# Optimization experiments

Hardware: AMD Instinct MI355X
Metric: run time of the kernel (lower is better)

The kernel has to match this reference:

```python
import jax, jax.numpy as jnp
import numpy as np

B, L, D, N = 2, 2048, 1024, 16
HD = D // N  # head_dim = 64
EPS = 1e-5


def layer_norm(x, gamma, beta):
    mu = jnp.mean(x, axis=-1, keepdims=True)
    var = jnp.mean(jnp.square(x - mu), axis=-1, keepdims=True)
    return (x - mu) * jax.lax.rsqrt(var + EPS) * gamma + beta


def setup_inputs() -> dict:
    key = jax.random.key(0)
    ks = jax.random.split(key, 10)
    s = lambda fan_in: 1.0 / np.sqrt(fan_in)
    return {
        "x": jax.random.normal(ks[0], (B, L, D), dtype=jnp.float32),
        "wq": jax.random.uniform(ks[1], (D, D), jnp.float32, -s(D), s(D)),
        "wk": jax.random.uniform(ks[2], (D, D), jnp.float32, -s(D), s(D)),  # shared w_proj (k and v)
        "wo": jax.random.uniform(ks[3], (D, D), jnp.float32, -s(D), s(D)),
        "g1": jnp.ones((D,), jnp.float32),
        "b1": jnp.zeros((D,), jnp.float32),
        "w1": jax.random.uniform(ks[4], (D, 4 * D), jnp.float32, -s(D), s(D)),
        "bb1": jax.random.uniform(ks[5], (4 * D,), jnp.float32, -s(D), s(D)),
        "w2": jax.random.uniform(ks[6], (4 * D, D), jnp.float32, -s(4 * D), s(4 * D)),
        "bb2": jax.random.uniform(ks[7], (D,), jnp.float32, -s(4 * D), s(4 * D)),
        "g2": jnp.ones((D,), jnp.float32),
        "b2": jnp.zeros((D,), jnp.float32),
    }


def reference(x, wq, wk, wo, g1, b1, w1, bb1, w2, bb2, g2, b2):
    b, l, d = x.shape
    # projections (w_proj is shared for k and v in the source; v output is unused)
    q = (x @ wq).reshape(b, l, HD, N)
    k = (x @ wk).reshape(b, l, HD, N)
    # attention scores [b, l, m, n]; softmax over m (dim=2 in source)
    scores = jnp.einsum('bldn,bmdn->blmn', q, k) / np.sqrt(HD).astype(np.float32)
    attn = jax.nn.softmax(scores, axis=2)
    # NOTE: source contracts attention weights with K, not V (faithful bug reproduction)
    ctx = jnp.einsum('blmn,bmdn->bldn', attn, k).reshape(b, l, d)
    attn_out = ctx @ wo
    # post-LN residual block
    h = layer_norm(x + attn_out, g1, b1)
    ff = jax.nn.gelu(h @ w1 + bb1, approximate=False) @ w2 + bb2
    return layer_norm(h + ff, g2, b2)
```

## Files before the change

### kernel.cpp

```cpp
#include <hip/hip_runtime.h>
#include <math.h>

typedef unsigned short u16;
typedef unsigned int u32;
typedef __bf16 bf16x8 __attribute__((ext_vector_type(8)));
typedef unsigned short us8 __attribute__((ext_vector_type(8)));
typedef unsigned short us4 __attribute__((ext_vector_type(4)));
typedef float f32x4 __attribute__((ext_vector_type(4)));

#define DEV __device__ __forceinline__

DEV float fast_exp2(float x) { return __builtin_amdgcn_exp2f(x); }

DEV u16 f2bf(float f) {
  __bf16 h = (__bf16)f;
  return __builtin_bit_cast(u16, h);
}
DEV float bf2f(u16 h) { return __builtin_bit_cast(float, (u32)h << 16); }

DEV bf16x8 ld_bf8(const u16* p) { return __builtin_bit_cast(bf16x8, *(const us8*)p); }

DEV void gload_lds16(const u16* g, u16* l) {
  __builtin_amdgcn_global_load_lds((const __attribute__((address_space(1))) void*)g,
                                   (__attribute__((address_space(3))) void*)l, 16, 0, 0);
}

DEV f32x4 mfma16(bf16x8 a, bf16x8 b, f32x4 c) {
  return __builtin_amdgcn_mfma_f32_16x16x32_bf16(a, b, c, 0, 0, 0);
}

DEV float fast_gelu(float u) {
  const float e = fast_exp2(-u * (2.3022048f + 0.10294343f * u * u));
  return u / (1.f + e);
}

#define BAR __builtin_amdgcn_s_barrier()
#define LGK asm volatile("s_waitcnt lgkmcnt(0)" ::: "memory")
#define VM4 asm volatile("s_waitcnt vmcnt(4)" ::: "memory")


__global__ void conv_bf16_kernel(const float* __restrict__ in, u16* __restrict__ out, int n4) {
  const int stride = gridDim.x * blockDim.x;
  for (int i = blockIdx.x * blockDim.x + threadIdx.x; i < n4; i += stride) {
    float4 v = ((const float4*)in)[i];
    us4 h; h[0] = f2bf(v.x); h[1] = f2bf(v.y); h[2] = f2bf(v.z); h[3] = f2bf(v.w);
    ((us4*)out)[i] = h;
  }
}

template <int P>
__global__ __launch_bounds__(256) void transpose_bf16_kernel(
    const float* __restrict__ in, u16* __restrict__ out, int K, int N, float scale) {
  __shared__ float tile[32][33];
  const int nbk = K >> 5;
  const int bk = blockIdx.x % nbk, bn = blockIdx.x / nbk;
  const int r0 = bk << 5, c0 = bn << 5;
  const int t = threadIdx.x;
  {
    const int r = t >> 3, c4 = (t & 7) << 2;
    int sr = r0 + r;
    if constexpr (P == 2) sr = ((sr & 63) << 4) | (sr >> 6);
    const float4 v = *(const float4*)(in + (size_t)sr * N + c0 + c4);
    tile[r][c4] = v.x; tile[r][c4 + 1] = v.y; tile[r][c4 + 2] = v.z; tile[r][c4 + 3] = v.w;
  }
  __syncthreads();
  {
    const int oc = t >> 3, r4 = (t & 7) << 2;
    int orow = c0 + oc;
    if constexpr (P == 1) orow = ((orow & 15) << 6) | (orow >> 4);
    us4 h;
#pragma unroll
    for (int j = 0; j < 4; j++) h[j] = f2bf(tile[r4 + j][oc] * scale);
    *(us4*)(out + (size_t)orow * K + r0 + r4) = h;
  }
}

__global__ __launch_bounds__(256) void khead_transpose(
    const u16* __restrict__ qk, u16* __restrict__ kth) {
  __shared__ u16 tT[64 * 64];
  char* base = (char*)tT;
  const int t = threadIdx.x;
  const int bid = blockIdx.x;
  const int lt = bid & 31, n = (bid >> 5) & 15, b = bid >> 9;
#pragma unroll
  for (int rr = 0; rr < 2; rr++) {
    const int l = rr * 32 + (t >> 3);
    const int d0 = (t & 7) * 8;
    us8 v = *(const us8*)(qk + ((size_t)(b * 2048 + lt * 64 + l)) * 2048 + 1024 + n * 64 + d0);
#pragma unroll
    for (int j = 0; j < 8; j++) {
      const int d = d0 + j;
      *(u16*)(base + d * 128 + ((2 * l) ^ (16 * (d >> 3)))) = v[j];
    }
  }
  __syncthreads();
  const int w = t >> 6, lane = t & 63;
#pragma unroll
  for (int rr = 0; rr < 2; rr++) {
    const int d = rr * 32 + w * 8 + (lane >> 3);
    const int l = (lane & 7) * 8;
    us8 v = *(const us8*)(base + d * 128 + ((2 * l) ^ (16 * (d >> 3))));
    *(us8*)(kth + ((size_t)((b * 16 + n) * 64 + d)) * 2048 + lt * 64 + l) = v;
  }
}

template <int MODE, int BN>
__global__ __launch_bounds__(256) void gemm128(
    const u16* __restrict__ A, const u16* __restrict__ BT,
    int M, int N, int K,
    u16* __restrict__ ob, float* __restrict__ of, const float* __restrict__ res) {
  constexpr int NJ = BN / 32;
  constexpr int WCC = BN / 2;
  __shared__ u16 As[2][4096];
  __shared__ u16 Bs[2][BN * 32];
  const int t = threadIdx.x;
  const int nbm = M >> 7;
  const int nblk = nbm * (N / BN);
  int bid = blockIdx.x;
  bid = (bid & 7) * (nblk >> 3) + (bid >> 3);
  const int bm = bid % nbm;
  const int bn = bid / nbm;
  const int m0 = bm << 7, n0 = bn * BN;
  const int w = t >> 6, lane = t & 63;
  const int wr = w >> 1, wc = w & 1;
  const int lr = lane & 15, lg = lane >> 4, lq = (lane >> 4) << 2;
  const int rsw = (lg ^ (lr & 3)) << 3;

  const int srow = t >> 2;
  const int sseg = (t & 3) ^ (srow & 3);
  const u16* ap = A + (size_t)(m0 + srow) * K + sseg * 8;
  const u16* bp = BT + (size_t)(n0 + srow) * K + sseg * 8;
  const size_t half = (size_t)64 * K;

#define STAGE(buf, k0)                                                 \
  {                                                                    \
    gload_lds16(ap + (k0), &As[buf][t << 3]);                          \
    gload_lds16(ap + half + (k0), &As[buf][(t << 3) + 2048]);          \
    gload_lds16(bp + (k0), &Bs[buf][t << 3]);                          \
    if constexpr (BN == 128)                                           \
      gload_lds16(bp + half + (k0), &Bs[buf][(t << 3) + 2048]);        \
  }

  f32x4 acc[4][NJ];
#pragma unroll
  for (int i = 0; i < 4; i++)
#pragma unroll
    for (int j = 0; j < NJ; j++) acc[i][j] = (f32x4){0.f, 0.f, 0.f, 0.f};

  STAGE(0, 0);
  __syncthreads();
  const int NI = K >> 5;
  for (int it = 0; it < NI; ++it) {
    const int buf = it & 1;
    if (it + 1 < NI) STAGE(buf ^ 1, (it + 1) << 5);
    bf16x8 af[4], bfr[NJ];
#pragma unroll
    for (int i = 0; i < 4; i++)
      af[i] = ld_bf8(&As[buf][(wr * 64 + i * 16 + lr) * 32 + rsw]);
#pragma unroll
    for (int j = 0; j < NJ; j++)
      bfr[j] = ld_bf8(&Bs[buf][(wc * WCC + j * 16 + lr) * 32 + rsw]);
#pragma unroll
    for (int i = 0; i < 4; i++)
#pragma unroll
      for (int j = 0; j < NJ; j++) acc[i][j] = mfma16(af[i], bfr[j], acc[i][j]);
    __syncthreads();
  }
#undef STAGE

#pragma unroll
  for (int i = 0; i < 4; i++) {
    const int r0 = m0 + wr * 64 + i * 16 + lq;
#pragma unroll
    for (int j = 0; j < NJ; j++) {
      const int c = n0 + wc * WCC + j * 16 + lr;
      if constexpr (MODE == 0) {
#pragma unroll
        for (int q = 0; q < 4; q++) ob[(size_t)(r0 + q) * N + c] = f2bf(acc[i][j][q]);
      } else {
#pragma unroll
        for (int q = 0; q < 4; q++) {
          const size_t idx = (size_t)(r0 + q) * N + c;
          of[idx] = acc[i][j][q] + res[idx];
        }
      }
    }
  }
}

template <int MODE, int KS>
__global__ __launch_bounds__(512, 2) void gemm256(
    const u16* __restrict__ A, const u16* __restrict__ BT,
    int M, int N, int K,
    u16* __restrict__ ob, float* __restrict__ of, const float* __restrict__ bias) {
  __shared__ u16 AL[2][2][8192];
  __shared__ u16 BL[2][2][8192];
  const int t = threadIdx.x;
  const int lane = t & 63, wid = t >> 6;
  const int lr = lane & 15, lg = lane >> 4;
  const int wm = wid >> 2, wn = wid & 3;
  const int nbm = M >> 8, nbn = N >> 8;
  const int nblk = nbm * nbn * KS;
  int bid = blockIdx.x;
  bid = (bid & 7) * (nblk >> 3) + (bid >> 3);
  int ks = 0;
  if constexpr (KS > 1) { ks = bid % KS; bid /= KS; }
  const int bm = bid % nbm, bn = bid / nbm;
  const int m0 = bm << 8, n0 = bn << 8;
  const int KB = K / KS;
  const int NT = KB >> 6;
  const u16* Ag = A + (size_t)m0 * K + ks * KB;
  const u16* Bg = BT + (size_t)n0 * K + ks * KB;
  const int sseg = (t & 7) ^ ((t >> 3) & 7);
  const int akey = lr & 7;

  auto stgA = [&](int buf, int h, int kt) {
    const u16* s = Ag + (size_t)(h * 128 + (t >> 3)) * K + kt * 64 + sseg * 8;
    gload_lds16(s, &AL[buf][h][t * 8]);
    gload_lds16(s + (size_t)64 * K, &AL[buf][h][4096 + t * 8]);
  };
  auto stgB = [&](int buf, int h, int kt) {
    const u16* s = Bg + (size_t)(h * 128 + (t >> 3)) * K + kt * 64 + sseg * 8;
    gload_lds16(s, &BL[buf][h][t * 8]);
    gload_lds16(s + (size_t)64 * K, &BL[buf][h][4096 + t * 8]);
  };

#define RDA(DST, BUF, IB)                                                      \
  _Pragma("unroll") for (int i4 = 0; i4 < 4; i4++)                             \
  _Pragma("unroll") for (int kk = 0; kk < 2; kk++)                             \
    DST[i4][kk] = ld_bf8(&AL[BUF][wm][((IB + i4) * 16 + lr) * 64 +             \
                                      ((kk * 4 + lg) ^ akey) * 8]);
#define RDB(DST, BUF, JB)                                                      \
  _Pragma("unroll") for (int j2 = 0; j2 < 2; j2++)                             \
  _Pragma("unroll") for (int kk = 0; kk < 2; kk++)                             \
    DST[j2][kk] = ld_bf8(&BL[BUF][wn >> 1][((wn & 1) * 64 + (JB + j2) * 16 +   \
                                            lr) * 64 +                         \
                                           ((kk * 4 + lg) ^ akey) * 8]);
#define QUAD(AF, BF, IB, JB)                                                   \
  __builtin_amdgcn_s_setprio(1);                                               \
  _Pragma("unroll") for (int i4 = 0; i4 < 4; i4++)                             \
  _Pragma("unroll") for (int j2 = 0; j2 < 2; j2++)                             \
  _Pragma("unroll") for (int kk = 0; kk < 2; kk++)                             \
    acc[IB + i4][JB + j2] = mfma16(AF[i4][kk], BF[j2][kk], acc[IB + i4][JB + j2]); \
  __builtin_amdgcn_s_setprio(0);

  f32x4 acc[8][4];
#pragma unroll
  for (int i = 0; i < 8; i++)
#pragma unroll
    for (int j = 0; j < 4; j++) acc[i][j] = (f32x4){0.f, 0.f, 0.f, 0.f};
  bf16x8 a0[4][2], a1[4][2], b0[2][2], b1[2][2];

  stgA(0, 0, 0); stgA(0, 1, 0); stgB(0, 0, 0); stgB(0, 1, 0);
  stgA(1, 0, 1); stgA(1, 1, 1);
  VM4;
  BAR;

  const int NI = NT >> 1;
  for (int it = 0; it < NI; ++it) {
    const int kt1 = 2 * it + 1;
    const int ktA = (2 * it + 2 < NT) ? 2 * it + 2 : NT - 1;
    const int ktB = (2 * it + 3 < NT) ? 2 * it + 3 : NT - 1;
    RDA(a0, 0, 0); RDB(b0, 0, 0); stgB(1, 0, kt1);
    BAR; QUAD(a0, b0, 0, 0); LGK; BAR;
    RDA(a1, 0, 4); stgB(1, 1, kt1);
    BAR; QUAD(a1, b0, 4, 0); LGK; BAR;
    RDB(b1, 0, 2); stgA(0, 0, ktA);
    BAR; QUAD(a1, b1, 4, 2); LGK; BAR;
    stgA(0, 1, ktA);
    BAR; QUAD(a0, b1, 0, 2); LGK; VM4; BAR;
    RDA(a0, 1, 0); RDB(b0, 1, 0); stgB(0, 0, ktA);
    BAR; QUAD(a0, b0, 0, 0); LGK; BAR;
    RDA(a1, 1, 4); stgB(0, 1, ktA);
    BAR; QUAD(a1, b0, 4, 0); LGK; BAR;
    RDB(b1, 1, 2); stgA(1, 0, ktB);
    BAR; QUAD(a1, b1, 4, 2); LGK; BAR;
    stgA(1, 1, ktB);
    BAR; QUAD(a0, b1, 0, 2); LGK; VM4; BAR;
  }
#undef RDA
#undef RDB
#undef QUAD

#pragma unroll
  for (int i = 0; i < 8; i++) {
    const int r = m0 + wm * 128 + i * 16 + lg * 4;
#pragma unroll
    for (int j = 0; j < 4; j++) {
      const int c = n0 + wn * 64 + j * 16 + lr;
      if constexpr (MODE == 0) {
        const float bv = bias[c];
#pragma unroll
        for (int q = 0; q < 4; q++)
          ob[(size_t)(r + q) * N + c] = f2bf(fast_gelu(acc[i][j][q] + bv));
      } else if constexpr (MODE == 1) {
        u16* op = ob + (size_t)ks * M * N;
#pragma unroll
        for (int q = 0; q < 4; q++) op[(size_t)(r + q) * N + c] = f2bf(acc[i][j][q]);
      } else {
#pragma unroll
        for (int q = 0; q < 4; q++) ob[(size_t)(r + q) * N + c] = f2bf(acc[i][j][q]);
      }
    }
  }
}

__global__ __launch_bounds__(256, 4) void attn_kernel(
    const u16* __restrict__ qk, const u16* __restrict__ kth,
    u16* __restrict__ op, float* __restrict__ stat) {
  __shared__ u16 KsB[2][4096];
  __shared__ u16 KtsB[2][4096];
  __shared__ u16 Plds[4][1024];
  const int t = threadIdx.x, w = t >> 6, lane = t & 63;
  const int lr = lane & 15, lg = lane >> 4;
  int bid = blockIdx.x;
  bid = (bid & 7) * 128 + (bid >> 3);
  const int kv = bid & 1, qb = (bid >> 1) & 15, hn = (bid >> 5) & 15, b = bid >> 9;
  const int lw = qb * 128 + w * 32;
  const int m00 = kv * 1024;
  const u16* ksrc = qk + (size_t)b * 2048 * 2048 + 1024 + hn * 64;
  const u16* ktb = kth + ((size_t)(b * 16 + hn)) * 64 * 2048;
  char* pb = (char*)&Plds[w][0];
  const int swz = (lr & 7) << 4;

#define STAGE_KV(buf, m0s)                                                    \
  {                                                                           \
    _Pragma("unroll") for (int i_ = 0; i_ < 2; i_++) {                        \
      const int s_ = t + 256 * i_;                                            \
      const int row_ = s_ >> 3;                                               \
      const int c_ = (s_ & 7) ^ (row_ & 7);                                   \
      gload_lds16(ksrc + (size_t)((m0s) + row_) * 2048 + c_ * 8,              \
                  &KsB[buf][s_ * 8]);                                         \
      gload_lds16(ktb + (size_t)row_ * 2048 + (m0s) + c_ * 8,                 \
                  &KtsB[buf][s_ * 8]);                                        \
    }                                                                         \
  }

  bf16x8 qf[2][2];
#pragma unroll
  for (int f = 0; f < 2; f++)
#pragma unroll
    for (int kk = 0; kk < 2; kk++)
      qf[f][kk] = ld_bf8(qk + (size_t)(b * 2048 + lw + 16 * f + lr) * 2048 + hn * 64 +
                         kk * 32 + lg * 8);

  float lrow[2] = {0.f, 0.f};
  f32x4 o[2][4];
#pragma unroll
  for (int f = 0; f < 2; f++)
#pragma unroll
    for (int dj = 0; dj < 4; dj++) o[f][dj] = (f32x4){0.f, 0.f, 0.f, 0.f};

  STAGE_KV(0, m00);
  __syncthreads();

  for (int it = 0; it < 16; ++it) {
    const int buf = it & 1;
    if (it < 15) STAGE_KV(buf ^ 1, m00 + (it + 1) * 64);

    f32x4 sc[2][4];
#pragma unroll
    for (int f = 0; f < 2; f++)
#pragma unroll
      for (int mj = 0; mj < 4; mj++) sc[f][mj] = (f32x4){0.f, 0.f, 0.f, 0.f};
#pragma unroll
    for (int mj = 0; mj < 4; mj++) {
      const int krow = 16 * mj + lr;
      bf16x8 kf0 = ld_bf8(&KsB[buf][krow * 64 + ((lg ^ (krow & 7)) << 3)]);
      bf16x8 kf1 = ld_bf8(&KsB[buf][krow * 64 + (((4 + lg) ^ (krow & 7)) << 3)]);
#pragma unroll
      for (int f = 0; f < 2; f++) {
        sc[f][mj] = mfma16(kf0, qf[f][0], sc[f][mj]);
        sc[f][mj] = mfma16(kf1, qf[f][1], sc[f][mj]);
      }
    }

    bf16x8 pa[2][2];
#pragma unroll
    for (int f = 0; f < 2; f++) {
      float ts = 0.f;
#pragma unroll
      for (int mj = 0; mj < 4; mj++) {
        float p0 = fast_exp2(sc[f][mj][0]);
        float p1 = fast_exp2(sc[f][mj][1]);
        float p2 = fast_exp2(sc[f][mj][2]);
        float p3 = fast_exp2(sc[f][mj][3]);
        ts += (p0 + p1) + (p2 + p3);
        u32 w0 = (u32)f2bf(p0) | ((u32)f2bf(p1) << 16);
        u32 w1 = (u32)f2bf(p2) | ((u32)f2bf(p3) << 16);
        *(uint2*)(pb + ((lr * 128 + mj * 32 + lg * 8) ^ swz)) = make_uint2(w0, w1);
      }
      lrow[f] += ts;
#pragma unroll
      for (int kk = 0; kk < 2; kk++)
        pa[f][kk] = __builtin_bit_cast(
            bf16x8, *(const us8*)(pb + ((lr * 128 + kk * 64 + lg * 16) ^ swz)));
    }

#pragma unroll
    for (int dj = 0; dj < 4; dj++) {
      const int vrow = dj * 16 + lr;
      bf16x8 v0 = ld_bf8(&KtsB[buf][vrow * 64 + ((lg ^ (vrow & 7)) << 3)]);
      bf16x8 v1 = ld_bf8(&KtsB[buf][vrow * 64 + (((4 + lg) ^ (vrow & 7)) << 3)]);
#pragma unroll
      for (int f = 0; f < 2; f++) {
        o[f][dj] = mfma16(pa[f][0], v0, o[f][dj]);
        o[f][dj] = mfma16(pa[f][1], v1, o[f][dj]);
      }
    }
    __syncthreads();
  }
#undef STAGE_KV

  u16* ob = op + (size_t)kv * 4096 * 1024;
#pragma unroll
  for (int f = 0; f < 2; f++) {
    lrow[f] += __shfl_xor(lrow[f], 16);
    lrow[f] += __shfl_xor(lrow[f], 32);
#pragma unroll
    for (int q = 0; q < 4; q++) {
      const int ll = lw + 16 * f + 4 * lg + q;
#pragma unroll
      for (int dj = 0; dj < 4; dj++) {
        ob[((size_t)(b * 2048 + ll)) * 1024 + hn * 64 + dj * 16 + lr] = f2bf(o[f][dj][q]);
      }
    }
    if (lg == 0) {
      const int sidx = (b * 16 + hn) * 2048 + lw + 16 * f + lr;
      stat[kv * 65536 + sidx] = lrow[f];
    }
  }
}

__global__ __launch_bounds__(256) void attn_combine(
    const u16* __restrict__ op, const float* __restrict__ stat, u16* __restrict__ ctxh) {
  const int row = blockIdx.x, t = threadIdx.x;
  const int hn = t >> 4;
  const int b = row >> 11, l = row & 2047;
  const int sidx = (b * 16 + hn) * 2048 + l;
  const float inv = 1.f / (stat[sidx] + stat[65536 + sidx]);
  const us4 a = *(const us4*)(op + (size_t)row * 1024 + t * 4);
  const us4 c = *(const us4*)(op + (size_t)(4096 + row) * 1024 + t * 4);
  us4 h;
#pragma unroll
  for (int j = 0; j < 4; j++) h[j] = f2bf((bf2f(a[j]) + bf2f(c[j])) * inv);
  *(us4*)(ctxh + (size_t)row * 1024 + t * 4) = h;
}

__global__ __launch_bounds__(256) void ln1_kernel(
    const float* __restrict__ in, const float* __restrict__ gamma,
    const float* __restrict__ beta, u16* __restrict__ o16) {
  __shared__ float red[8];
  const int row = blockIdx.x, t = threadIdx.x;
  const float4 v = ((const float4*)(in + (size_t)row * 1024))[t];
  float s = v.x + v.y + v.z + v.w;
  float ss = v.x * v.x + v.y * v.y + v.z * v.z + v.w * v.w;
#pragma unroll
  for (int off = 1; off < 64; off <<= 1) { s += __shfl_xor(s, off); ss += __shfl_xor(ss, off); }
  if ((t & 63) == 0) { red[t >> 6] = s; red[4 + (t >> 6)] = ss; }
  __syncthreads();
  const float st = red[0] + red[1] + red[2] + red[3];
  const float sst = red[4] + red[5] + red[6] + red[7];
  const float mean = st * (1.f / 1024.f);
  const float var = sst * (1.f / 1024.f) - mean * mean;
  const float rs = rsqrtf(var + 1e-5f);
  const float4 gv = ((const float4*)gamma)[t];
  const float4 bv = ((const float4*)beta)[t];
  us4 h;
  h[0] = f2bf((v.x - mean) * rs * gv.x + bv.x);
  h[1] = f2bf((v.y - mean) * rs * gv.y + bv.y);
  h[2] = f2bf((v.z - mean) * rs * gv.z + bv.z);
  h[3] = f2bf((v.w - mean) * rs * gv.w + bv.w);
  *(us4*)(o16 + (size_t)row * 1024 + t * 4) = h;
}

template <int NP>
__global__ __launch_bounds__(256) void ln2_kernel(
    const u16* __restrict__ p, size_t pstride,
    const u16* __restrict__ resb, const float* __restrict__ bias,
    const float* __restrict__ gamma, const float* __restrict__ beta,
    float* __restrict__ o32) {
  __shared__ float red[8];
  const int row = blockIdx.x, t = threadIdx.x;
  float4 v;
  {
    const float4 vb = ((const float4*)bias)[t];
    const us4 rb = *(const us4*)(resb + (size_t)row * 1024 + t * 4);
    v.x = bf2f(rb[0]) + vb.x;
    v.y = bf2f(rb[1]) + vb.y;
    v.z = bf2f(rb[2]) + vb.z;
    v.w = bf2f(rb[3]) + vb.w;
  }
#pragma unroll
  for (int k = 0; k < NP; k++) {
    const us4 pv = *(const us4*)(p + (size_t)k * pstride + (size_t)row * 1024 + t * 4);
    v.x += bf2f(pv[0]); v.y += bf2f(pv[1]); v.z += bf2f(pv[2]); v.w += bf2f(pv[3]);
  }
  float s = v.x + v.y + v.z + v.w;
  float ss = v.x * v.x + v.y * v.y + v.z * v.z + v.w * v.w;
#pragma unroll
  for (int off = 1; off < 64; off <<= 1) { s += __shfl_xor(s, off); ss += __shfl_xor(ss, off); }
  if ((t & 63) == 0) { red[t >> 6] = s; red[4 + (t >> 6)] = ss; }
  __syncthreads();
  const float st = red[0] + red[1] + red[2] + red[3];
  const float sst = red[4] + red[5] + red[6] + red[7];
  const float mean = st * (1.f / 1024.f);
  const float var = sst * (1.f / 1024.f) - mean * mean;
  const float rs = rsqrtf(var + 1e-5f);
  const float4 gv = ((const float4*)gamma)[t];
  const float4 bv = ((const float4*)beta)[t];
  float4 ov;
  ov.x = (v.x - mean) * rs * gv.x + bv.x;
  ov.y = (v.y - mean) * rs * gv.y + bv.y;
  ov.z = (v.z - mean) * rs * gv.z + bv.z;
  ov.w = (v.w - mean) * rs * gv.w + bv.w;
  ((float4*)(o32 + (size_t)row * 1024))[t] = ov;
}

extern "C" void kernel_launch(void* const* d_in, const int* in_sizes, int n_in,
                              void* d_out, int out_size, void* d_ws, size_t ws_size,
                              hipStream_t stream) {
  const float* x   = (const float*)d_in[0];
  const float* wq  = (const float*)d_in[1];
  const float* wk  = (const float*)d_in[2];
  const float* wo  = (const float*)d_in[3];
  const float* g1  = (const float*)d_in[4];
  const float* b1  = (const float*)d_in[5];
  const float* w1  = (const float*)d_in[6];
  const float* bb1 = (const float*)d_in[7];
  const float* w2  = (const float*)d_in[8];
  const float* bb2 = (const float*)d_in[9];
  const float* g2  = (const float*)d_in[10];
  const float* b2  = (const float*)d_in[11];

  char* ws = (char*)d_ws;
  const size_t MB = 1ull << 20;
  u16* w2T   = (u16*)(ws + 0 * MB);
  u16* hb    = (u16*)(ws + 8 * MB);
  u16* obuf  = (u16*)(ws + 16 * MB);
  float* stat = (float*)(ws + 32 * MB);
  u16* tbuf  = (u16*)(ws + 16 * MB);
  u16* rA16  = (u16*)(ws + 48 * MB);
  u16* wqkT  = (u16*)(ws + 26 * MB);
  u16* xb    = (u16*)(ws + 33 * MB);
  u16* qk    = (u16*)(ws + 41 * MB);
  u16* kthp  = (u16*)(ws + 57 * MB);
  u16* ctxh  = (u16*)(ws + 65 * MB);
  float* rbuf = (float*)(ws + 73 * MB);
  u16* w1T   = (u16*)(ws + 89 * MB);
  u16* woT   = (u16*)(ws + 97 * MB);

  conv_bf16_kernel<<<1024, 256, 0, stream>>>(x, xb, 1048576);
  transpose_bf16_kernel<1><<<1024, 256, 0, stream>>>(wq, wqkT, 1024, 1024, 0.125f * 1.44269504089f);
  transpose_bf16_kernel<1><<<1024, 256, 0, stream>>>(wk, wqkT + (size_t)1024 * 1024, 1024, 1024, 1.0f);
  transpose_bf16_kernel<2><<<1024, 256, 0, stream>>>(wo, woT, 1024, 1024, 1.0f);
  transpose_bf16_kernel<0><<<32 * 128, 256, 0, stream>>>(w1, w1T, 1024, 4096, 1.0f);
  transpose_bf16_kernel<0><<<128 * 32, 256, 0, stream>>>(w2, w2T, 4096, 1024, 1.0f);

  gemm256<2, 1><<<128, 512, 0, stream>>>(xb, wqkT, 4096, 2048, 1024, qk, nullptr, nullptr);
  khead_transpose<<<1024, 256, 0, stream>>>(qk, kthp);

  attn_kernel<<<1024, 256, 0, stream>>>(qk, kthp, obuf, stat);
  attn_combine<<<4096, 256, 0, stream>>>(obuf, stat, ctxh);

  gemm128<2, 64><<<32 * 16, 256, 0, stream>>>(ctxh, woT, 4096, 1024, 1024, nullptr, rbuf, x);
  ln1_kernel<<<4096, 256, 0, stream>>>(rbuf, g1, b1, hb);

  gemm256<0, 1><<<256, 512, 0, stream>>>(hb, w1T, 4096, 4096, 1024, tbuf, nullptr, bb1);
  const size_t MN = (size_t)4096 * 1024;
  gemm256<1, 4><<<256, 512, 0, stream>>>(tbuf, w2T, 4096, 1024, 4096, rA16, nullptr, nullptr);
  ln2_kernel<4><<<4096, 256, 0, stream>>>(rA16, MN, hb, bb2, g2, b2, (float*)d_out);
}
```

Before: 243.1 us.

## Split-K QK and Wo GEMMs, fold partial sums into consumers, MFMA row sums

The QK projection GEMM now uses 2-way split-K with bf16 partials, which khead_transpose and attn_kernel sum on load. khead_transpose also writes a contiguous per-head K copy. The Wo GEMM moves from the 128-tile kernel to the 256-tile kernel with 4-way split-K, and ln1 sums the partials plus the fp32 residual. Attention row sums are computed with an MFMA against a ones vector instead of scalar adds and shuffles, and priority hints bracket the MFMA sections. The aim is better GPU occupancy on small-grid GEMMs, at the cost of extra partial-buffer traffic and bf16 rounding of the partials.

```diff
diff --git a/kernel.cpp b/kernel.cpp
--- a/kernel.cpp
+++ b/kernel.cpp
@@ -76,9 +76,10 @@
 }
 
 __global__ __launch_bounds__(256) void khead_transpose(
-    const u16* __restrict__ qk, u16* __restrict__ kth) {
+    const u16* __restrict__ qkP, u16* __restrict__ kth, u16* __restrict__ ksum) {
   __shared__ u16 tT[64 * 64];
   char* base = (char*)tT;
+  const size_t PS = (size_t)4096 * 2048;
   const int t = threadIdx.x;
   const int bid = blockIdx.x;
   const int lt = bid & 31, n = (bid >> 5) & 15, b = bid >> 9;
@@ -86,11 +87,17 @@
   for (int rr = 0; rr < 2; rr++) {
     const int l = rr * 32 + (t >> 3);
     const int d0 = (t & 7) * 8;
-    us8 v = *(const us8*)(qk + ((size_t)(b * 2048 + lt * 64 + l)) * 2048 + 1024 + n * 64 + d0);
+    const size_t idx = ((size_t)(b * 2048 + lt * 64 + l)) * 2048 + 1024 + n * 64 + d0;
+    us8 va = *(const us8*)(qkP + idx);
+    us8 vb = *(const us8*)(qkP + PS + idx);
+    us8 sm;
+#pragma unroll
+    for (int j = 0; j < 8; j++) sm[j] = f2bf(bf2f(va[j]) + bf2f(vb[j]));
+    *(us8*)(ksum + (((size_t)(b * 16 + n) * 2048 + lt * 64 + l)) * 64 + d0) = sm;
 #pragma unroll
     for (int j = 0; j < 8; j++) {
       const int d = d0 + j;
-      *(u16*)(base + d * 128 + ((2 * l) ^ (16 * (d >> 3)))) = v[j];
+      *(u16*)(base + d * 128 + ((2 * l) ^ (16 * (d >> 3)))) = sm[j];
     }
   }
   __syncthreads();
@@ -104,95 +111,11 @@
   }
 }
 
-template <int MODE, int BN>
-__global__ __launch_bounds__(256) void gemm128(
-    const u16* __restrict__ A, const u16* __restrict__ BT,
-    int M, int N, int K,
-    u16* __restrict__ ob, float* __restrict__ of, const float* __restrict__ res) {
-  constexpr int NJ = BN / 32;
-  constexpr int WCC = BN / 2;
-  __shared__ u16 As[2][4096];
-  __shared__ u16 Bs[2][BN * 32];
-  const int t = threadIdx.x;
-  const int nbm = M >> 7;
-  const int nblk = nbm * (N / BN);
-  int bid = blockIdx.x;
-  bid = (bid & 7) * (nblk >> 3) + (bid >> 3);
-  const int bm = bid % nbm;
-  const int bn = bid / nbm;
-  const int m0 = bm << 7, n0 = bn * BN;
-  const int w = t >> 6, lane = t & 63;
-  const int wr = w >> 1, wc = w & 1;
-  const int lr = lane & 15, lg = lane >> 4, lq = (lane >> 4) << 2;
-  const int rsw = (lg ^ (lr & 3)) << 3;
-
-  const int srow = t >> 2;
-  const int sseg = (t & 3) ^ (srow & 3);
-  const u16* ap = A + (size_t)(m0 + srow) * K + sseg * 8;
-  const u16* bp = BT + (size_t)(n0 + srow) * K + sseg * 8;
-  const size_t half = (size_t)64 * K;
-
-#define STAGE(buf, k0)                                                 \
-  {                                                                    \
-    gload_lds16(ap + (k0), &As[buf][t << 3]);                          \
-    gload_lds16(ap + half + (k0), &As[buf][(t << 3) + 2048]);          \
-    gload_lds16(bp + (k0), &Bs[buf][t << 3]);                          \
-    if constexpr (BN == 128)                                           \
-      gload_lds16(bp + half + (k0), &Bs[buf][(t << 3) + 2048]);        \
-  }
-
-  f32x4 acc[4][NJ];
-#pragma unroll
-  for (int i = 0; i < 4; i++)
-#pragma unroll
-    for (int j = 0; j < NJ; j++) acc[i][j] = (f32x4){0.f, 0.f, 0.f, 0.f};
-
-  STAGE(0, 0);
-  __syncthreads();
-  const int NI = K >> 5;
-  for (int it = 0; it < NI; ++it) {
-    const int buf = it & 1;
-    if (it + 1 < NI) STAGE(buf ^ 1, (it + 1) << 5);
-    bf16x8 af[4], bfr[NJ];
-#pragma unroll
-    for (int i = 0; i < 4; i++)
-      af[i] = ld_bf8(&As[buf][(wr * 64 + i * 16 + lr) * 32 + rsw]);
-#pragma unroll
-    for (int j = 0; j < NJ; j++)
-      bfr[j] = ld_bf8(&Bs[buf][(wc * WCC + j * 16 + lr) * 32 + rsw]);
-#pragma unroll
-    for (int i = 0; i < 4; i++)
-#pragma unroll
-      for (int j = 0; j < NJ; j++) acc[i][j] = mfma16(af[i], bfr[j], acc[i][j]);
-    __syncthreads();
-  }
-#undef STAGE
-
-#pragma unroll
-  for (int i = 0; i < 4; i++) {
-    const int r0 = m0 + wr * 64 + i * 16 + lq;
-#pragma unroll
-    for (int j = 0; j < NJ; j++) {
-      const int c = n0 + wc * WCC + j * 16 + lr;
-      if constexpr (MODE == 0) {
-#pragma unroll
-        for (int q = 0; q < 4; q++) ob[(size_t)(r0 + q) * N + c] = f2bf(acc[i][j][q]);
-      } else {
-#pragma unroll
-        for (int q = 0; q < 4; q++) {
-          const size_t idx = (size_t)(r0 + q) * N + c;
-          of[idx] = acc[i][j][q] + res[idx];
-        }
-      }
-    }
-  }
-}
-
 template <int MODE, int KS>
 __global__ __launch_bounds__(512, 2) void gemm256(
     const u16* __restrict__ A, const u16* __restrict__ BT,
     int M, int N, int K,
-    u16* __restrict__ ob, float* __restrict__ of, const float* __restrict__ bias) {
+    u16* __restrict__ ob, const float* __restrict__ bias) {
   __shared__ u16 AL[2][2][8192];
   __shared__ u16 BL[2][2][8192];
   const int t = threadIdx.x;
@@ -293,24 +216,22 @@
 #pragma unroll
         for (int q = 0; q < 4; q++)
           ob[(size_t)(r + q) * N + c] = f2bf(fast_gelu(acc[i][j][q] + bv));
-      } else if constexpr (MODE == 1) {
+      } else {
         u16* op = ob + (size_t)ks * M * N;
 #pragma unroll
         for (int q = 0; q < 4; q++) op[(size_t)(r + q) * N + c] = f2bf(acc[i][j][q]);
-      } else {
-#pragma unroll
-        for (int q = 0; q < 4; q++) ob[(size_t)(r + q) * N + c] = f2bf(acc[i][j][q]);
       }
     }
   }
 }
 
 __global__ __launch_bounds__(256, 4) void attn_kernel(
-    const u16* __restrict__ qk, const u16* __restrict__ kth,
-    u16* __restrict__ op, float* __restrict__ stat) {
+    const u16* __restrict__ qkP, const u16* __restrict__ ksum,
+    const u16* __restrict__ kth, u16* __restrict__ op, float* __restrict__ stat) {
   __shared__ u16 KsB[2][4096];
   __shared__ u16 KtsB[2][4096];
   __shared__ u16 Plds[4][1024];
+  const size_t PS = (size_t)4096 * 2048;
   const int t = threadIdx.x, w = t >> 6, lane = t & 63;
   const int lr = lane & 15, lg = lane >> 4;
   int bid = blockIdx.x;
@@ -318,7 +239,7 @@
   const int kv = bid & 1, qb = (bid >> 1) & 15, hn = (bid >> 5) & 15, b = bid >> 9;
   const int lw = qb * 128 + w * 32;
   const int m00 = kv * 1024;
-  const u16* ksrc = qk + (size_t)b * 2048 * 2048 + 1024 + hn * 64;
+  const u16* ksrc = ksum + ((size_t)(b * 16 + hn)) * 2048 * 64;
   const u16* ktb = kth + ((size_t)(b * 16 + hn)) * 64 * 2048;
   char* pb = (char*)&Plds[w][0];
   const int swz = (lr & 7) << 4;
@@ -329,7 +250,7 @@
       const int s_ = t + 256 * i_;                                            \
       const int row_ = s_ >> 3;                                               \
       const int c_ = (s_ & 7) ^ (row_ & 7);                                   \
-      gload_lds16(ksrc + (size_t)((m0s) + row_) * 2048 + c_ * 8,              \
+      gload_lds16(ksrc + (size_t)((m0s) + row_) * 64 + c_ * 8,                \
                   &KsB[buf][s_ * 8]);                                         \
       gload_lds16(ktb + (size_t)row_ * 2048 + (m0s) + c_ * 8,                 \
                   &KtsB[buf][s_ * 8]);                                        \
@@ -340,16 +261,30 @@
 #pragma unroll
   for (int f = 0; f < 2; f++)
 #pragma unroll
-    for (int kk = 0; kk < 2; kk++)
-      qf[f][kk] = ld_bf8(qk + (size_t)(b * 2048 + lw + 16 * f + lr) * 2048 + hn * 64 +
-                         kk * 32 + lg * 8);
-
-  float lrow[2] = {0.f, 0.f};
+    for (int kk = 0; kk < 2; kk++) {
+      const size_t qi = (size_t)(b * 2048 + lw + 16 * f + lr) * 2048 + hn * 64 +
+                        kk * 32 + lg * 8;
+      us8 qa = *(const us8*)(qkP + qi);
+      us8 qb2 = *(const us8*)(qkP + PS + qi);
+      us8 qs;
+#pragma unroll
+      for (int j = 0; j < 8; j++) qs[j] = f2bf(bf2f(qa[j]) + bf2f(qb2[j]));
+      qf[f][kk] = __builtin_bit_cast(bf16x8, qs);
+    }
+
+  us8 ou;
+#pragma unroll
+  for (int j = 0; j < 8; j++) ou[j] = 0x3f80;
+  const bf16x8 ones = __builtin_bit_cast(bf16x8, ou);
+
+  f32x4 ol[2];
   f32x4 o[2][4];
 #pragma unroll
-  for (int f = 0; f < 2; f++)
+  for (int f = 0; f < 2; f++) {
+    ol[f] = (f32x4){0.f, 0.f, 0.f, 0.f};
 #pragma unroll
     for (int dj = 0; dj < 4; dj++) o[f][dj] = (f32x4){0.f, 0.f, 0.f, 0.f};
+  }
 
   STAGE_KV(0, m00);
   __syncthreads();
@@ -363,6 +298,7 @@
     for (int f = 0; f < 2; f++)
 #pragma unroll
       for (int mj = 0; mj < 4; mj++) sc[f][mj] = (f32x4){0.f, 0.f, 0.f, 0.f};
+    __builtin_amdgcn_s_setprio(1);
 #pragma unroll
     for (int mj = 0; mj < 4; mj++) {
       const int krow = 16 * mj + lr;
@@ -374,29 +310,30 @@
         sc[f][mj] = mfma16(kf1, qf[f][1], sc[f][mj]);
       }
     }
+    __builtin_amdgcn_s_setprio(0);
 
     bf16x8 pa[2][2];
 #pragma unroll
     for (int f = 0; f < 2; f++) {
-      float ts = 0.f;
 #pragma unroll
       for (int mj = 0; mj < 4; mj++) {
         float p0 = fast_exp2(sc[f][mj][0]);
         float p1 = fast_exp2(sc[f][mj][1]);
         float p2 = fast_exp2(sc[f][mj][2]);
         float p3 = fast_exp2(sc[f][mj][3]);
-        ts += (p0 + p1) + (p2 + p3);
         u32 w0 = (u32)f2bf(p0) | ((u32)f2bf(p1) << 16);
         u32 w1 = (u32)f2bf(p2) | ((u32)f2bf(p3) << 16);
         *(uint2*)(pb + ((lr * 128 + mj * 32 + lg * 8) ^ swz)) = make_uint2(w0, w1);
       }
-      lrow[f] += ts;
 #pragma unroll
       for (int kk = 0; kk < 2; kk++)
         pa[f][kk] = __builtin_bit_cast(
             bf16x8, *(const us8*)(pb + ((lr * 128 + kk * 64 + lg * 16) ^ swz)));
-    }
-
+      ol[f] = mfma16(pa[f][0], ones, ol[f]);
+      ol[f] = mfma16(pa[f][1], ones, ol[f]);
+    }
+
+    __builtin_amdgcn_s_setprio(1);
 #pragma unroll
     for (int dj = 0; dj < 4; dj++) {
       const int vrow = dj * 16 + lr;
@@ -408,6 +345,7 @@
         o[f][dj] = mfma16(pa[f][1], v1, o[f][dj]);
       }
     }
+    __builtin_amdgcn_s_setprio(0);
     __syncthreads();
   }
 #undef STAGE_KV
@@ -415,8 +353,6 @@
   u16* ob = op + (size_t)kv * 4096 * 1024;
 #pragma unroll
   for (int f = 0; f < 2; f++) {
-    lrow[f] += __shfl_xor(lrow[f], 16);
-    lrow[f] += __shfl_xor(lrow[f], 32);
 #pragma unroll
     for (int q = 0; q < 4; q++) {
       const int ll = lw + 16 * f + 4 * lg + q;
@@ -425,9 +361,10 @@
         ob[((size_t)(b * 2048 + ll)) * 1024 + hn * 64 + dj * 16 + lr] = f2bf(o[f][dj][q]);
       }
     }
-    if (lg == 0) {
-      const int sidx = (b * 16 + hn) * 2048 + lw + 16 * f + lr;
-      stat[kv * 65536 + sidx] = lrow[f];
+    if (lr == 0) {
+      const int sb = (b * 16 + hn) * 2048 + lw + 16 * f + 4 * lg;
+#pragma unroll
+      for (int q = 0; q < 4; q++) stat[kv * 65536 + sb + q] = ol[f][q];
     }
   }
 }
@@ -448,11 +385,17 @@
 }
 
 __global__ __launch_bounds__(256) void ln1_kernel(
-    const float* __restrict__ in, const float* __restrict__ gamma,
-    const float* __restrict__ beta, u16* __restrict__ o16) {
+    const u16* __restrict__ p, size_t pstride, const float* __restrict__ xres,
+    const float* __restrict__ gamma, const float* __restrict__ beta,
+    u16* __restrict__ o16) {
   __shared__ float red[8];
   const int row = blockIdx.x, t = threadIdx.x;
-  const float4 v = ((const float4*)(in + (size_t)row * 1024))[t];
+  float4 v = ((const float4*)(xres + (size_t)row * 1024))[t];
+#pragma unroll
+  for (int k = 0; k < 4; k++) {
+    const us4 pv = *(const us4*)(p + (size_t)k * pstride + (size_t)row * 1024 + t * 4);
+    v.x += bf2f(pv[0]); v.y += bf2f(pv[1]); v.z += bf2f(pv[2]); v.w += bf2f(pv[3]);
+  }
   float s = v.x + v.y + v.z + v.w;
   float ss = v.x * v.x + v.y * v.y + v.z * v.z + v.w * v.w;
 #pragma unroll
@@ -474,7 +417,6 @@
   *(us4*)(o16 + (size_t)row * 1024 + t * 4) = h;
 }
 
-template <int NP>
 __global__ __launch_bounds__(256) void ln2_kernel(
     const u16* __restrict__ p, size_t pstride,
     const u16* __restrict__ resb, const float* __restrict__ bias,
@@ -492,7 +434,7 @@
     v.w = bf2f(rb[3]) + vb.w;
   }
 #pragma unroll
-  for (int k = 0; k < NP; k++) {
+  for (int k = 0; k < 4; k++) {
     const us4 pv = *(const us4*)(p + (size_t)k * pstride + (size_t)row * 1024 + t * 4);
     v.x += bf2f(pv[0]); v.y += bf2f(pv[1]); v.z += bf2f(pv[2]); v.w += bf2f(pv[3]);
   }
@@ -537,16 +479,17 @@
   const size_t MB = 1ull << 20;
   u16* w2T   = (u16*)(ws + 0 * MB);
   u16* hb    = (u16*)(ws + 8 * MB);
-  u16* obuf  = (u16*)(ws + 16 * MB);
-  float* stat = (float*)(ws + 32 * MB);
+  u16* qkP   = (u16*)(ws + 16 * MB);
   u16* tbuf  = (u16*)(ws + 16 * MB);
+  u16* obuf  = (u16*)(ws + 48 * MB);
+  float* stat = (float*)(ws + 64 * MB);
+  u16* woP   = (u16*)(ws + 48 * MB);
   u16* rA16  = (u16*)(ws + 48 * MB);
-  u16* wqkT  = (u16*)(ws + 26 * MB);
-  u16* xb    = (u16*)(ws + 33 * MB);
-  u16* qk    = (u16*)(ws + 41 * MB);
-  u16* kthp  = (u16*)(ws + 57 * MB);
-  u16* ctxh  = (u16*)(ws + 65 * MB);
-  float* rbuf = (float*)(ws + 73 * MB);
+  u16* xb    = (u16*)(ws + 65 * MB);
+  u16* ksum  = (u16*)(ws + 65 * MB);
+  u16* kthp  = (u16*)(ws + 73 * MB);
+  u16* wqkT  = (u16*)(ws + 81 * MB);
+  u16* ctxh  = (u16*)(ws + 81 * MB);
   u16* w1T   = (u16*)(ws + 89 * MB);
   u16* woT   = (u16*)(ws + 97 * MB);
 
@@ -557,17 +500,17 @@
   transpose_bf16_kernel<0><<<32 * 128, 256, 0, stream>>>(w1, w1T, 1024, 4096, 1.0f);
   transpose_bf16_kernel<0><<<128 * 32, 256, 0, stream>>>(w2, w2T, 4096, 1024, 1.0f);
 
-  gemm256<2, 1><<<128, 512, 0, stream>>>(xb, wqkT, 4096, 2048, 1024, qk, nullptr, nullptr);
-  khead_transpose<<<1024, 256, 0, stream>>>(qk, kthp);
-
-  attn_kernel<<<1024, 256, 0, stream>>>(qk, kthp, obuf, stat);
+  gemm256<1, 2><<<256, 512, 0, stream>>>(xb, wqkT, 4096, 2048, 1024, qkP, nullptr);
+  khead_transpose<<<1024, 256, 0, stream>>>(qkP, kthp, ksum);
+
+  attn_kernel<<<1024, 256, 0, stream>>>(qkP, ksum, kthp, obuf, stat);
   attn_combine<<<4096, 256, 0, stream>>>(obuf, stat, ctxh);
 
-  gemm128<2, 64><<<32 * 16, 256, 0, stream>>>(ctxh, woT, 4096, 1024, 1024, nullptr, rbuf, x);
-  ln1_kernel<<<4096, 256, 0, stream>>>(rbuf, g1, b1, hb);
-
-  gemm256<0, 1><<<256, 512, 0, stream>>>(hb, w1T, 4096, 4096, 1024, tbuf, nullptr, bb1);
+  gemm256<1, 4><<<256, 512, 0, stream>>>(ctxh, woT, 4096, 1024, 1024, woP, nullptr);
   const size_t MN = (size_t)4096 * 1024;
-  gemm256<1, 4><<<256, 512, 0, stream>>>(tbuf, w2T, 4096, 1024, 4096, rA16, nullptr, nullptr);
-  ln2_kernel<4><<<4096, 256, 0, stream>>>(rA16, MN, hb, bb2, g2, b2, (float*)d_out);
-}
+  ln1_kernel<<<4096, 256, 0, stream>>>(woP, MN, x, g1, b1, hb);
+
+  gemm256<0, 1><<<256, 512, 0, stream>>>(hb, w1T, 4096, 4096, 1024, tbuf, bb1);
+  gemm256<1, 4><<<256, 512, 0, stream>>>(tbuf, w2T, 4096, 1024, 4096, rA16, nullptr);
+  ln2_kernel<<<4096, 256, 0, stream>>>(rA16, MN, hb, bb2, g2, b2, (float*)d_out);
+}
```

Result: faster. 237.3 us (-2.4%).
